# Optimization experiments

Measured on AMD Instinct MI355X. Metric: run time of the kernel, lower is better.

The kernel has to match this reference:

```python
import jax, jax.numpy as jnp
import numpy as np


def setup_inputs() -> dict:
    key = jax.random.key(0)
    ks = jax.random.split(key, 8)
    C, G, F = 500, 200, 500          # cells_oi, genes_oi, position bins (fragmentprob_size)
    N_GENES, N_CLUST = 1000, 10      # total genes, clusters
    NFRAG = 5_000_000
    bincounts = jax.random.randint(ks[0], (G, F), 0, 20).astype(jnp.float32)
    baseline_weight = jax.random.normal(ks[1], (N_GENES, F), jnp.float32) * 0.1
    differential_weight = jax.random.normal(ks[2], (N_CLUST, 1, 1), jnp.float32) * 0.01
    cluster_modifier = jax.random.normal(ks[3], (N_CLUST,), jnp.float32) * 0.01
    genes_oi = jax.random.randint(ks[4], (G,), 0, N_GENES)
    labels = jax.random.randint(ks[5], (C,), 0, N_CLUST)
    local_cellxgene_ix = jax.random.randint(ks[6], (NFRAG,), 0, C * G)
    binix = jax.random.randint(ks[7], (NFRAG,), 0, F)
    return dict(bincounts=bincounts, baseline_weight=baseline_weight,
                differential_weight=differential_weight, cluster_modifier=cluster_modifier,
                genes_oi=genes_oi, labels=labels,
                local_cellxgene_ix=local_cellxgene_ix, binix=binix)


def reference(bincounts, baseline_weight, differential_weight, cluster_modifier,
              genes_oi, labels, local_cellxgene_ix, binix):
    G, F = bincounts.shape
    C = labels.shape[0]
    # predictor2 is Identity, final_channels = n_hidden_dims = 1
    gene_embedding = bincounts[:, :, None]                     # [G, F, 1]
    baseline = baseline_weight[genes_oi]                       # [G, F]
    cell_embedding = differential_weight[labels][:, :, 0]      # [C, 1]
    # matmul([1,G,F,H], [C,1,H,1]).squeeze(-1) -> [C,G,F]
    u = (jnp.einsum('gfh,ch->cgf', gene_embedding, cell_embedding)
         + baseline[None]
         + cluster_modifier[labels][:, None, None])            # [C, G, F]
    # histogram of fragments into (cell x gene x bin)
    idx = local_cellxgene_ix * F + binix
    count = jnp.zeros(C * G * F, dtype=u.dtype).at[idx].add(1.0).reshape(C, G, F)
    # Poisson(rate=exp(u)).log_prob(count) = count*u - exp(u) - lgamma(count+1)
    logp = count * u - jnp.exp(u) - jax.lax.lgamma(count + 1.0)
    return logp.sum(-1)                                        # [C, G]
```

## Files before the change

### kernel.cpp

```cpp
#include <hip/hip_runtime.h>
#include <stdint.h>

#define C_   500
#define G_   200
#define F_   500
#define K_   10
#define CG_  (C_ * G_)
#define CGPB 128
#define NBUCK ((CG_ + CGPB - 1) / CGPB)
#define WPRW 64
#define NCW  (CGPB * WPRW)
#define TPB_P 1024
#define GRID_P 512
#define NBLK 512
#define TPB_B 512
#define CHUNK_MAX 10240
#define FPT2 (CHUNK_MAX / TPB_P / 2)
#define SLOT 32
#define OVF_CAP 32
#define LN2F 0.69314718f

__constant__ float LGF[16] = {
    0.0f, 0.0f, 0.69314718f, 1.79175947f, 3.17805383f, 4.78749174f,
    6.57925121f, 8.52516136f, 10.60460290f, 12.80182748f, 15.10441257f,
    17.50230785f, 19.98721450f, 22.55216385f, 25.19122118f, 27.89927138f
};

__global__ __launch_bounds__(TPB_P) void partition_kernel(
        const int* __restrict__ lci,
        const int* __restrict__ binix,
        const float* __restrict__ bc,
        const float* __restrict__ bw,
        const int* __restrict__ genes_oi,
        const float* __restrict__ dw,
        const float* __restrict__ cm,
        uint16_t* __restrict__ frag16,
        uint16_t* __restrict__ cnt16,
        uint32_t* __restrict__ ovfn,
        uint32_t* __restrict__ ovfe,
        float* __restrict__ u_tab,
        float* __restrict__ E,
        int NF, int chunk) {
    __shared__ uint16_t smem16[NBUCK * SLOT];
    __shared__ uint32_t hist[NBUCK];
    __shared__ float    psum[4];
    __shared__ uint32_t ovf_lds[OVF_CAP];
    __shared__ uint32_t oc;
    int tid = threadIdx.x;
    int blk = blockIdx.x;
    int s0 = blk * chunk;
    int s1 = min(s0 + chunk, NF);
    int nloc = s1 - s0;

    if (tid < NBUCK) hist[tid] = 0;
    if (tid < 4) psum[tid] = 0.0f;
    if (tid == 0) oc = 0u;
    __syncthreads();

    {
        int p = blk * 4 + (tid >> 8);
        if (p < K_ * G_) {
            int sub = tid & 255;
            int k = p / G_;
            int g = p - k * G_;
            float dwk = dw[k];
            float cmk = cm[k];
            const float* bcg = bc + (size_t)g * F_;
            const float* bwg = bw + (size_t)genes_oi[g] * F_;
            float* urow = u_tab + (size_t)p * F_;
            float u0 = dwk * bcg[sub] + bwg[sub] + cmk;
            urow[sub] = u0;
            float s = __expf(u0);
            int f1 = sub + 256;
            if (f1 < F_) {
                float u1 = dwk * bcg[f1] + bwg[f1] + cmk;
                urow[f1] = u1;
                s += __expf(u1);
            }
#pragma unroll
            for (int off = 32; off > 0; off >>= 1) s += __shfl_down(s, off);
            if ((tid & 63) == 0) atomicAdd(&psum[tid >> 8], s);
        }
    }

    const int2* lci2 = (const int2*)(lci + s0);
    const int2* bin2 = (const int2*)(binix + s0);

    auto frag = [&](uint32_t cg, uint32_t f) {
        uint32_t b  = cg >> 7;
        uint32_t lp = ((cg & 127u) << 9) | f;
        uint32_t r  = atomicAdd(&hist[b], 1u);
        if (r < SLOT) smem16[b * SLOT + r] = (uint16_t)lp;
        else {
            uint32_t o = atomicAdd(&oc, 1u);
            if (o < OVF_CAP) ovf_lds[o] = (b << 16) | lp;
        }
    };

    if (nloc >= 2 * 4 * TPB_P) {
#pragma unroll
        for (int u = 0; u < 4; ++u) {
            int pi = u * TPB_P + tid;
            int2 cg2 = lci2[pi];
            int2 f2  = bin2[pi];
            frag((uint32_t)cg2.x, (uint32_t)f2.x);
            frag((uint32_t)cg2.y, (uint32_t)f2.y);
        }
        {
            int pi = 4 * TPB_P + tid;
            int e0 = pi * 2;
            if (e0 + 1 < nloc) {
                int2 cg2 = lci2[pi];
                int2 f2  = bin2[pi];
                frag((uint32_t)cg2.x, (uint32_t)f2.x);
                frag((uint32_t)cg2.y, (uint32_t)f2.y);
            } else if (e0 < nloc) {
                frag((uint32_t)lci[s0 + e0], (uint32_t)binix[s0 + e0]);
            }
        }
    } else {
#pragma unroll
        for (int u = 0; u < FPT2; ++u) {
            int pi = u * TPB_P + tid;
            int e0 = pi * 2;
            if (e0 + 1 < nloc) {
                int2 cg2 = lci2[pi];
                int2 f2  = bin2[pi];
                frag((uint32_t)cg2.x, (uint32_t)f2.x);
                frag((uint32_t)cg2.y, (uint32_t)f2.y);
            } else if (e0 < nloc) {
                frag((uint32_t)lci[s0 + e0], (uint32_t)binix[s0 + e0]);
            }
        }
    }
    __syncthreads();

    if (tid < 4) {
        int p = blk * 4 + tid;
        if (p < K_ * G_) E[p] = psum[tid];
    }
    if (tid < NBUCK)
        cnt16[(size_t)blk * NBUCK + tid] = (uint16_t)min(hist[tid], (uint32_t)SLOT);

    const uint4* s4 = (const uint4*)smem16;
    for (int i = tid; i < NBUCK * 4; i += TPB_P) {
        int seg = i >> 2;
        int q   = i & 3;
        uint32_t n = min(hist[seg], (uint32_t)SLOT);
        if ((uint32_t)(q * 8) < n) {
            uint4* dst = (uint4*)(frag16 + ((size_t)seg * NBLK + blk) * SLOT);
            dst[q] = s4[i];
        }
    }

    if (tid == 0) ovfn[blk] = min(oc, (uint32_t)OVF_CAP);
    if (tid < OVF_CAP && tid < oc) ovfe[blk * OVF_CAP + tid] = ovf_lds[tid];
}

__global__ __launch_bounds__(TPB_B) void bucket_kernel(
        const uint16_t* __restrict__ frag16,
        const uint16_t* __restrict__ cnt16,
        const uint32_t* __restrict__ ovfn,
        const uint32_t* __restrict__ ovfe,
        const float* __restrict__ u_tab,
        const float* __restrict__ E,
        const int* __restrict__ labels,
        float* __restrict__ out) {
    __shared__ uint32_t cnt[NCW];
    __shared__ uint16_t cnts[NBLK];
    __shared__ int pairidx[CGPB];
    int b = blockIdx.x;
    int tid = threadIdx.x;

    uint4* c4 = (uint4*)cnt;
    for (int w = tid; w < NCW / 4; w += TPB_B) c4[w] = make_uint4(0u, 0u, 0u, 0u);
    if (tid < CGPB) {
        int cg = b * CGPB + tid;
        if (cg < CG_) {
            int c = cg / G_;
            int g = cg - c * G_;
            pairidx[tid] = labels[c] * G_ + g;
        } else {
            pairidx[tid] = 0;
        }
    }
    if (tid < NBLK) cnts[tid] = cnt16[(size_t)tid * NBUCK + b];
    __syncthreads();

    const uint4* fb4 = (const uint4*)(frag16 + (size_t)b * NBLK * SLOT);
    for (int i = tid; i < NBLK * 4; i += TPB_B) {
        uint32_t blkq = (uint32_t)i >> 2;
        uint32_t q    = (uint32_t)i & 3u;
        int n  = (int)cnts[blkq];
        int j0 = (int)q * 8;
        if (j0 < n) {
            uint4 four = fb4[i];
            int m = n - j0;
            uint32_t wq[4] = {four.x, four.y, four.z, four.w};
#pragma unroll
            for (int t = 0; t < 8; ++t) {
                if (t < m) {
                    uint32_t l = (wq[t >> 1] >> ((t & 1) * 16)) & 0xFFFFu;
                    atomicAdd(&cnt[l >> 3], 1u << ((l & 7u) * 4u));
                }
            }
        }
    }
    if (tid < NBLK) {
        uint32_t on = ovfn[tid];
        for (uint32_t q = 0; q < on; ++q) {
            uint32_t e = ovfe[tid * OVF_CAP + q];
            if ((e >> 16) == (uint32_t)b) {
                uint32_t l = e & 0xFFFFu;
                atomicAdd(&cnt[l >> 3], 1u << ((l & 7u) * 4u));
            }
        }
    }
    __syncthreads();

    int wave = tid >> 6, lane = tid & 63;
    for (int r = wave; r < CGPB; r += (TPB_B / 64)) {
        int cg = b * CGPB + r;
        if (cg >= CG_) break;
        float s = 0.0f;
        if (lane < 63) {
            uint32_t v = cnt[r * WPRW + lane];
            if (v) {
                const float4* up = (const float4*)(u_tab + (size_t)pairidx[r] * F_ + 8 * lane);
                float4 ua = up[0];
                float4 ub = up[1];
                s += (float)( v        & 0xFu) * ua.x
                   + (float)((v >> 4)  & 0xFu) * ua.y
                   + (float)((v >> 8)  & 0xFu) * ua.z
                   + (float)((v >> 12) & 0xFu) * ua.w
                   + (float)((v >> 16) & 0xFu) * ub.x
                   + (float)((v >> 20) & 0xFu) * ub.y
                   + (float)((v >> 24) & 0xFu) * ub.z
                   + (float)((v >> 28)       ) * ub.w;
                if (v & 0xEEEEEEEEu) {
#pragma unroll
                    for (int q = 0; q < 8; ++q)
                        s -= LGF[(v >> (q * 4)) & 0xFu];
                }
            }
        }
#pragma unroll
        for (int off = 32; off > 0; off >>= 1) s += __shfl_down(s, off);
        if (lane == 0) out[cg] = s - E[pairidx[r]];
    }
}

extern "C" void kernel_launch(void* const* d_in, const int* in_sizes, int n_in,
                              void* d_out, int out_size, void* d_ws, size_t ws_size,
                              hipStream_t stream) {
    const float* bc     = (const float*)d_in[0];
    const float* bw     = (const float*)d_in[1];
    const float* dw     = (const float*)d_in[2];
    const float* cm     = (const float*)d_in[3];
    const int* genes_oi = (const int*)d_in[4];
    const int* labels   = (const int*)d_in[5];
    const int* lci      = (const int*)d_in[6];
    const int* binix    = (const int*)d_in[7];
    float* out = (float*)d_out;

    const int NF = in_sizes[6];
    int chunk = (NF + GRID_P - 1) / GRID_P;
    chunk = (chunk + 1) & ~1;
    if (chunk > CHUNK_MAX) chunk = CHUNK_MAX;

    char* ws = (char*)d_ws;
    size_t off_cnt16 = ((size_t)NBUCK * NBLK * SLOT * sizeof(uint16_t) + 255) & ~(size_t)255;
    size_t off_ovfn  = (off_cnt16 + (size_t)NBLK * NBUCK * sizeof(uint16_t) + 255) & ~(size_t)255;
    size_t off_ovfe  = (off_ovfn + NBLK * sizeof(uint32_t) + 255) & ~(size_t)255;
    size_t off_utab  = (off_ovfe + (size_t)NBLK * OVF_CAP * sizeof(uint32_t) + 255) & ~(size_t)255;
    size_t off_E     = (off_utab + ((size_t)K_ * G_ * F_ + 16) * sizeof(float) + 255) & ~(size_t)255;

    uint16_t* frag16 = (uint16_t*)ws;
    uint16_t* cnt16  = (uint16_t*)(ws + off_cnt16);
    uint32_t* ovfn   = (uint32_t*)(ws + off_ovfn);
    uint32_t* ovfe   = (uint32_t*)(ws + off_ovfe);
    float*    u_tab  = (float*)(ws + off_utab);
    float*    E      = (float*)(ws + off_E);

    partition_kernel<<<GRID_P, TPB_P, 0, stream>>>(
        lci, binix, bc, bw, genes_oi, dw, cm,
        frag16, cnt16, ovfn, ovfe, u_tab, E, NF, chunk);

    bucket_kernel<<<NBUCK, TPB_B, 0, stream>>>(
        frag16, cnt16, ovfn, ovfe, u_tab, E, labels, out);
}
```

Baseline: 126.0 us.

## Halve bucket size and embed per-segment counts in fragment slot headers

Buckets now cover 64 cell-gene pairs instead of 128, so there are twice as many bucket blocks, each with a smaller LDS count table and 256 threads. Each 16-entry segment stores its own fragment count in the first halfword, which removes the separate cnt16 array and its strided gather in the bucket kernel. The intent is better occupancy and parallelism in the bucket stage, plus less scattered metadata traffic. In exchange, per-segment capacity drops to 15, so more fragments may take the overflow path, and that path is capped at 32 entries per block.

```diff
diff --git a/kernel.cpp b/kernel.cpp
--- a/kernel.cpp
+++ b/kernel.cpp
@@ -6,17 +6,18 @@
 #define F_   500
 #define K_   10
 #define CG_  (C_ * G_)
-#define CGPB 128
+#define CGPB 64
 #define NBUCK ((CG_ + CGPB - 1) / CGPB)
 #define WPRW 64
 #define NCW  (CGPB * WPRW)
 #define TPB_P 1024
 #define GRID_P 512
 #define NBLK 512
-#define TPB_B 512
+#define TPB_B 256
 #define CHUNK_MAX 10240
 #define FPT2 (CHUNK_MAX / TPB_P / 2)
-#define SLOT 32
+#define SEGW 16
+#define PAY  15
 #define OVF_CAP 32
 #define LN2F 0.69314718f
 
@@ -35,13 +36,12 @@
         const float* __restrict__ dw,
         const float* __restrict__ cm,
         uint16_t* __restrict__ frag16,
-        uint16_t* __restrict__ cnt16,
         uint32_t* __restrict__ ovfn,
         uint32_t* __restrict__ ovfe,
         float* __restrict__ u_tab,
         float* __restrict__ E,
         int NF, int chunk) {
-    __shared__ uint16_t smem16[NBUCK * SLOT];
+    __shared__ uint16_t smem16[NBUCK * SEGW];
     __shared__ uint32_t hist[NBUCK];
     __shared__ float    psum[4];
     __shared__ uint32_t ovf_lds[OVF_CAP];
@@ -52,7 +52,7 @@
     int s1 = min(s0 + chunk, NF);
     int nloc = s1 - s0;
 
-    if (tid < NBUCK) hist[tid] = 0;
+    for (int i = tid; i < NBUCK; i += TPB_P) hist[i] = 0;
     if (tid < 4) psum[tid] = 0.0f;
     if (tid == 0) oc = 0u;
     __syncthreads();
@@ -87,10 +87,10 @@
     const int2* bin2 = (const int2*)(binix + s0);
 
     auto frag = [&](uint32_t cg, uint32_t f) {
-        uint32_t b  = cg >> 7;
-        uint32_t lp = ((cg & 127u) << 9) | f;
+        uint32_t b  = cg >> 6;
+        uint32_t lp = ((cg & 63u) << 9) | f;
         uint32_t r  = atomicAdd(&hist[b], 1u);
-        if (r < SLOT) smem16[b * SLOT + r] = (uint16_t)lp;
+        if (r < PAY) smem16[b * SEGW + 1 + r] = (uint16_t)lp;
         else {
             uint32_t o = atomicAdd(&oc, 1u);
             if (o < OVF_CAP) ovf_lds[o] = (b << 16) | lp;
@@ -139,17 +139,19 @@
         int p = blk * 4 + tid;
         if (p < K_ * G_) E[p] = psum[tid];
     }
-    if (tid < NBUCK)
-        cnt16[(size_t)blk * NBUCK + tid] = (uint16_t)min(hist[tid], (uint32_t)SLOT);
 
     const uint4* s4 = (const uint4*)smem16;
-    for (int i = tid; i < NBUCK * 4; i += TPB_P) {
-        int seg = i >> 2;
-        int q   = i & 3;
-        uint32_t n = min(hist[seg], (uint32_t)SLOT);
-        if ((uint32_t)(q * 8) < n) {
-            uint4* dst = (uint4*)(frag16 + ((size_t)seg * NBLK + blk) * SLOT);
-            dst[q] = s4[i];
+    for (int i = tid; i < NBUCK * 2; i += TPB_P) {
+        int seg = i >> 1;
+        int q   = i & 1;
+        uint32_t n = min(hist[seg], (uint32_t)PAY);
+        uint4* dst = (uint4*)(frag16 + ((size_t)seg * NBLK + blk) * SEGW);
+        if (q == 0) {
+            uint4 v = s4[seg * 2];
+            v.x = (v.x & 0xFFFF0000u) | n;
+            dst[0] = v;
+        } else if (n > 7) {
+            dst[1] = s4[seg * 2 + 1];
         }
     }
 
@@ -157,9 +159,8 @@
     if (tid < OVF_CAP && tid < oc) ovfe[blk * OVF_CAP + tid] = ovf_lds[tid];
 }
 
-__global__ __launch_bounds__(TPB_B) void bucket_kernel(
+__global__ __launch_bounds__(TPB_B, 8) void bucket_kernel(
         const uint16_t* __restrict__ frag16,
-        const uint16_t* __restrict__ cnt16,
         const uint32_t* __restrict__ ovfn,
         const uint32_t* __restrict__ ovfe,
         const float* __restrict__ u_tab,
@@ -167,7 +168,6 @@
         const int* __restrict__ labels,
         float* __restrict__ out) {
     __shared__ uint32_t cnt[NCW];
-    __shared__ uint16_t cnts[NBLK];
     __shared__ int pairidx[CGPB];
     int b = blockIdx.x;
     int tid = threadIdx.x;
@@ -184,32 +184,40 @@
             pairidx[tid] = 0;
         }
     }
-    if (tid < NBLK) cnts[tid] = cnt16[(size_t)tid * NBUCK + b];
-    __syncthreads();
-
-    const uint4* fb4 = (const uint4*)(frag16 + (size_t)b * NBLK * SLOT);
-    for (int i = tid; i < NBLK * 4; i += TPB_B) {
-        uint32_t blkq = (uint32_t)i >> 2;
-        uint32_t q    = (uint32_t)i & 3u;
-        int n  = (int)cnts[blkq];
-        int j0 = (int)q * 8;
-        if (j0 < n) {
-            uint4 four = fb4[i];
-            int m = n - j0;
-            uint32_t wq[4] = {four.x, four.y, four.z, four.w};
-#pragma unroll
-            for (int t = 0; t < 8; ++t) {
-                if (t < m) {
+    __syncthreads();
+
+    const uint4* fb4 = (const uint4*)(frag16 + (size_t)b * NBLK * SEGW);
+    for (int s = tid; s < NBLK; s += TPB_B) {
+        uint4 q0 = fb4[s * 2];
+        int n = (int)(q0.x & 0xFFFFu);
+        if (n > 0) {
+            int m1 = n < 7 ? n : 7;
+            uint32_t wq[4] = {q0.x, q0.y, q0.z, q0.w};
+#pragma unroll
+            for (int t = 1; t <= 7; ++t) {
+                if (t <= m1) {
                     uint32_t l = (wq[t >> 1] >> ((t & 1) * 16)) & 0xFFFFu;
                     atomicAdd(&cnt[l >> 3], 1u << ((l & 7u) * 4u));
                 }
             }
-        }
-    }
-    if (tid < NBLK) {
-        uint32_t on = ovfn[tid];
+            if (n > 7) {
+                uint4 q1 = fb4[s * 2 + 1];
+                int m2 = (n < PAY ? n : PAY) - 7;
+                uint32_t wr[4] = {q1.x, q1.y, q1.z, q1.w};
+#pragma unroll
+                for (int t = 0; t < 8; ++t) {
+                    if (t < m2) {
+                        uint32_t l = (wr[t >> 1] >> ((t & 1) * 16)) & 0xFFFFu;
+                        atomicAdd(&cnt[l >> 3], 1u << ((l & 7u) * 4u));
+                    }
+                }
+            }
+        }
+    }
+    for (int t = tid; t < NBLK; t += TPB_B) {
+        uint32_t on = ovfn[t];
         for (uint32_t q = 0; q < on; ++q) {
-            uint32_t e = ovfe[tid * OVF_CAP + q];
+            uint32_t e = ovfe[t * OVF_CAP + q];
             if ((e >> 16) == (uint32_t)b) {
                 uint32_t l = e & 0xFFFFu;
                 atomicAdd(&cnt[l >> 3], 1u << ((l & 7u) * 4u));
@@ -224,7 +232,7 @@
         if (cg >= CG_) break;
         float s = 0.0f;
         if (lane < 63) {
-            uint32_t v = cnt[r * WPRW + lane];
+            uint32_t v = cnt[(r << 6) + lane];
             if (v) {
                 const float4* up = (const float4*)(u_tab + (size_t)pairidx[r] * F_ + 8 * lane);
                 float4 ua = up[0];
@@ -269,14 +277,12 @@
     if (chunk > CHUNK_MAX) chunk = CHUNK_MAX;
 
     char* ws = (char*)d_ws;
-    size_t off_cnt16 = ((size_t)NBUCK * NBLK * SLOT * sizeof(uint16_t) + 255) & ~(size_t)255;
-    size_t off_ovfn  = (off_cnt16 + (size_t)NBLK * NBUCK * sizeof(uint16_t) + 255) & ~(size_t)255;
+    size_t off_ovfn  = ((size_t)NBUCK * NBLK * SEGW * sizeof(uint16_t) + 255) & ~(size_t)255;
     size_t off_ovfe  = (off_ovfn + NBLK * sizeof(uint32_t) + 255) & ~(size_t)255;
     size_t off_utab  = (off_ovfe + (size_t)NBLK * OVF_CAP * sizeof(uint32_t) + 255) & ~(size_t)255;
     size_t off_E     = (off_utab + ((size_t)K_ * G_ * F_ + 16) * sizeof(float) + 255) & ~(size_t)255;
 
     uint16_t* frag16 = (uint16_t*)ws;
-    uint16_t* cnt16  = (uint16_t*)(ws + off_cnt16);
     uint32_t* ovfn   = (uint32_t*)(ws + off_ovfn);
     uint32_t* ovfe   = (uint32_t*)(ws + off_ovfe);
     float*    u_tab  = (float*)(ws + off_utab);
@@ -284,8 +290,8 @@
 
     partition_kernel<<<GRID_P, TPB_P, 0, stream>>>(
         lci, binix, bc, bw, genes_oi, dw, cm,
-        frag16, cnt16, ovfn, ovfe, u_tab, E, NF, chunk);
+        frag16, ovfn, ovfe, u_tab, E, NF, chunk);
 
     bucket_kernel<<<NBUCK, TPB_B, 0, stream>>>(
-        frag16, cnt16, ovfn, ovfe, u_tab, E, labels, out);
+        frag16, ovfn, ovfe, u_tab, E, labels, out);
 }
```

Result: slower. 135.2 us (+7.3%).
